# Kernel optimization log

Measured on AMD Instinct MI355X. Metric: run time of the kernel, lower is better.

The kernel has to match this reference:

```python
import jax, jax.numpy as jnp
import numpy as np

N, L, H, D = 4, 2048, 16, 32   # batch, seq len, heads, projection_dim
DIM = H * D                     # 512 model dim


def setup_inputs() -> dict:
    rng = jax.random.key(0)
    k1, k2, k3, k4, k5 = jax.random.split(rng, 5)
    query = jax.random.normal(k1, (N, L, DIM), dtype=jnp.float32)
    key = jax.random.normal(k2, (N, L, DIM), dtype=jnp.float32)
    scale = 0.02
    Wq = jax.random.normal(k3, (DIM, DIM), dtype=jnp.float32) * scale
    Wk = jax.random.normal(k4, (DIM, DIM), dtype=jnp.float32) * scale
    Wv = jax.random.normal(k5, (DIM, DIM), dtype=jnp.float32) * scale
    return {"query": query, "key": key, "Wq": Wq, "Wk": Wk, "Wv": Wv, "mask": 1}


def reference(query, key, Wq, Wk, Wv, mask):
    # torch Linear(bias=False): y = x @ W^T
    n, Lq, _ = query.shape
    _, Lk, _ = key.shape
    q = (query @ Wq.T).reshape(n, Lq, H, D).transpose(0, 2, 1, 3)  # (N,H,Lq,D)
    k = (key @ Wk.T).reshape(n, Lk, H, D).transpose(0, 2, 1, 3)    # (N,H,Lk,D)
    v = (key @ Wv.T).reshape(n, Lk, H, D).transpose(0, 2, 1, 3)    # (N,H,Lk,D)
    q = jax.nn.softmax(q, axis=-1)
    k = jax.nn.softmax(k, axis=-1)
    # causal branch (mask truthy): Lq*Lk > D^2*Lk, so the module takes the
    # cumsum-of-outer-products ("right") path:
    #   right = cumsum_l( k_l outer v_l );  out_l = q_l @ right_l
    kv = jnp.einsum('nhld,nhle->nhlde', k, v)   # (N,H,Lk,D,D) outer products
    S = jnp.cumsum(kv, axis=2)                  # running prefix state
    out = jnp.einsum('nhld,nhlde->nhle', q, S)  # (N,H,Lq,D)
    return out.transpose(0, 2, 1, 3).reshape(n, Lq, H * D)
```

## Files before the change

kernel.cpp:

```cpp
#include <hip/hip_runtime.h>

#define NB      4
#define L_SEQ   2048
#define H_HEADS 16
#define D32     32
#define DIM     512
#define NH      (NB * H_HEADS)
#define CHUNK   64
#define NCHUNK  (L_SEQ / CHUNK)

typedef __attribute__((ext_vector_type(8))) short bf16x8;
typedef __attribute__((ext_vector_type(4))) float f32x4;

__device__ __forceinline__ unsigned short f2bf(float x) {
    unsigned u = __float_as_uint(x);
    u += 0x7fff + ((u >> 16) & 1);
    return (unsigned short)(u >> 16);
}
__device__ __forceinline__ unsigned pack2(float lo, float hi) {
    return (unsigned)f2bf(lo) | ((unsigned)f2bf(hi) << 16);
}

#define QN  4194304
#define WN  262144
#define TOT (2*QN + 3*WN)
__global__ __launch_bounds__(256) void convert_kernel(
    const float* __restrict__ query, const float* __restrict__ key,
    const float* __restrict__ Wq, const float* __restrict__ Wk,
    const float* __restrict__ Wv, unsigned short* __restrict__ dst)
{
    int idx = (blockIdx.x * 256 + threadIdx.x) * 8;
    const float* src; int off;
    if (idx < QN)               { src = query; off = idx; }
    else if (idx < 2*QN)        { src = key;   off = idx - QN; }
    else if (idx < 2*QN + WN)   { src = Wq;    off = idx - 2*QN; }
    else if (idx < 2*QN + 2*WN) { src = Wk;    off = idx - 2*QN - WN; }
    else                        { src = Wv;    off = idx - 2*QN - 2*WN; }
    float4 a = *(const float4*)(src + off);
    float4 b = *(const float4*)(src + off + 4);
    *(uint4*)(dst + idx) = make_uint4(pack2(a.x, a.y), pack2(a.z, a.w),
                                      pack2(b.x, b.y), pack2(b.z, b.w));
}

#define GLL(g, l) __builtin_amdgcn_global_load_lds( \
    (const __attribute__((address_space(1))) unsigned int*)(g), \
    (__attribute__((address_space(3))) unsigned int*)(l), 16, 0, 0)

__global__ __launch_bounds__(256) void gemm3_mfma_kernel(
    const unsigned short* __restrict__ qb, const unsigned short* __restrict__ kb2,
    const unsigned short* __restrict__ wqb, const unsigned short* __restrict__ wkb,
    const unsigned short* __restrict__ wvb,
    unsigned short* __restrict__ Qs, unsigned short* __restrict__ Ks,
    unsigned short* __restrict__ Vt)
{
    const int z  = blockIdx.z;
    const int bx = blockIdx.x >> 6;
    const int by = blockIdx.x & 63;
    const unsigned short *PA, *PB;
    int m0, n0;
    if (z == 0)      { PA = qb;  PB = wqb; m0 = by*128; n0 = bx*128; }
    else if (z == 1) { PA = kb2; PB = wkb; m0 = by*128; n0 = bx*128; }
    else             { PA = wvb; PB = kb2; m0 = bx*128; n0 = by*128; }

    __shared__ unsigned short Asm[3 * 4096];
    __shared__ unsigned short Bsm[3 * 4096];

    const int t    = threadIdx.x;
    const int w    = t >> 6;
    const int lane = t & 63;
    const int wm   = w >> 1, wn = w & 1;
    const int lm   = lane & 15, quad = lane >> 4;

    const int qswz = quad ^ ((lm >> 1) & 3);
    const int aoff = (wm * 64 + lm) * 32 + qswz * 8;
    const int boff = (wn * 64 + lm) * 32 + qswz * 8;

    const int li0 = t, li1 = t + 256;
    const int row0 = li0 >> 2, row1 = li1 >> 2;
    const int qs0 = (li0 & 3) ^ ((li0 >> 3) & 3);
    const int qs1 = (li1 & 3) ^ ((li1 >> 3) & 3);
    const unsigned short* gA0 = PA + (size_t)(m0 + row0) * DIM + qs0 * 8;
    const unsigned short* gA1 = PA + (size_t)(m0 + row1) * DIM + qs1 * 8;
    const unsigned short* gB0 = PB + (size_t)(n0 + row0) * DIM + qs0 * 8;
    const unsigned short* gB1 = PB + (size_t)(n0 + row1) * DIM + qs1 * 8;

    f32x4 acc[4][4] = {};

#define STAGE(buf, kb) do { \
    GLL(gA0 + (kb), Asm + (buf) * 4096 + li0 * 8); \
    GLL(gB0 + (kb), Bsm + (buf) * 4096 + li0 * 8); \
    GLL(gA1 + (kb), Asm + (buf) * 4096 + li1 * 8); \
    GLL(gB1 + (kb), Bsm + (buf) * 4096 + li1 * 8); \
} while (0)

    STAGE(0, 0);
    STAGE(1, 32);
    __builtin_amdgcn_sched_barrier(0);
    asm volatile("s_waitcnt vmcnt(4)" ::: "memory");
    __builtin_amdgcn_s_barrier();
    __builtin_amdgcn_sched_barrier(0);

    #pragma unroll
    for (int step = 0; step < 16; ++step) {
        const int cur = step % 3;
        if (step < 14) STAGE((step + 2) % 3, (step + 2) * 32);
        const unsigned short* As = Asm + cur * 4096;
        const unsigned short* Bs = Bsm + cur * 4096;
        bf16x8 af[4], bfr[4];
        #pragma unroll
        for (int i = 0; i < 4; i++)
            af[i] = *(const bf16x8*)(As + aoff + i * 512);
        #pragma unroll
        for (int j = 0; j < 4; j++)
            bfr[j] = *(const bf16x8*)(Bs + boff + j * 512);
        #pragma unroll
        for (int i = 0; i < 4; i++)
            #pragma unroll
            for (int j = 0; j < 4; j++)
                acc[i][j] = __builtin_amdgcn_mfma_f32_16x16x32_bf16(
                    af[i], bfr[j], acc[i][j], 0, 0, 0);
        __builtin_amdgcn_sched_barrier(0);
        if (step < 14)       asm volatile("s_waitcnt vmcnt(4)" ::: "memory");
        else if (step == 14) asm volatile("s_waitcnt vmcnt(0)" ::: "memory");
        if (step < 15) {
            __builtin_amdgcn_s_barrier();
            __builtin_amdgcn_sched_barrier(0);
        }
    }
#undef STAGE

    if (z < 2) {
        #pragma unroll
        for (int i = 0; i < 4; i++)
            #pragma unroll
            for (int jp = 0; jp < 2; jp++)
                #pragma unroll
                for (int r = 0; r < 4; r++) {
                    float a = acc[i][2 * jp][r], b = acc[i][2 * jp + 1][r];
                    float m = fmaxf(a, b);
                    #pragma unroll
                    for (int off = 1; off < 16; off <<= 1)
                        m = fmaxf(m, __shfl_xor(m, off, 64));
                    float ea = __expf(a - m), eb = __expf(b - m);
                    float s = ea + eb;
                    #pragma unroll
                    for (int off = 1; off < 16; off <<= 1)
                        s += __shfl_xor(s, off, 64);
                    float inv = 1.0f / s;
                    acc[i][2 * jp][r]     = ea * inv;
                    acc[i][2 * jp + 1][r] = eb * inv;
                }
    }

    #pragma unroll
    for (int i = 0; i < 4; i++) {
        int rbase = m0 + wm * 64 + i * 16 + quad * 4;
        #pragma unroll
        for (int r = 0; r < 4; r++) {
            int rg = rbase + r;
            #pragma unroll
            for (int j = 0; j < 4; j++) {
                int cg = n0 + wn * 64 + j * 16 + lm;
                unsigned short val = f2bf(acc[i][j][r]);
                if (z < 2) {
                    int n = rg >> 11, l = rg & 2047;
                    int h = cg >> 5,  e = cg & 31;
                    unsigned short* dp = (z == 0) ? Qs : Ks;
                    dp[(((size_t)(n * H_HEADS + h)) * L_SEQ + l) * D32 + e] = val;
                } else {
                    int h = rg >> 5,  e = rg & 31;
                    int n = cg >> 11, l = cg & 2047;
                    Vt[(((size_t)(n * H_HEADS + h)) * D32 + e) * L_SEQ + l] = val;
                }
            }
        }
    }
}

__global__ __launch_bounds__(64) void chunk_kv_mfma_kernel(
    const unsigned short* __restrict__ Ks, const unsigned short* __restrict__ Vt,
    float* __restrict__ ckvT)
{
    const int c = blockIdx.x, nh = blockIdx.y;
    const int lane = threadIdx.x;
    const int lm = lane & 15, quad = lane >> 4;

    __shared__ unsigned short Kl[64 * 36];

    {
        const unsigned short* kg = Ks + ((size_t)nh * L_SEQ + c * CHUNK + lane) * D32;
        #pragma unroll
        for (int i = 0; i < 4; i++) {
            uint4 v = *(const uint4*)(kg + i * 8);
            *(uint4*)(Kl + lane * 36 + i * 8) = v;
        }
    }
    __syncthreads();

    f32x4 acc[2][2] = {};
    #pragma unroll
    for (int ch = 0; ch < 2; ch++) {
        bf16x8 aV[2], bK[2];
        #pragma unroll
        for (int mt = 0; mt < 2; mt++)
            aV[mt] = *(const bf16x8*)(Vt + ((size_t)nh * D32 + mt * 16 + lm) * L_SEQ
                                         + c * CHUNK + ch * 32 + quad * 8);
        #pragma unroll
        for (int nt = 0; nt < 2; nt++) {
            const unsigned short* kp = Kl + (ch * 32 + quad * 8) * 36 + nt * 16 + lm;
            #pragma unroll
            for (int j = 0; j < 8; j++) bK[nt][j] = (short)kp[j * 36];
        }
        #pragma unroll
        for (int mt = 0; mt < 2; mt++)
            #pragma unroll
            for (int nt = 0; nt < 2; nt++)
                acc[mt][nt] = __builtin_amdgcn_mfma_f32_16x16x32_bf16(
                    aV[mt], bK[nt], acc[mt][nt], 0, 0, 0);
    }
    #pragma unroll
    for (int mt = 0; mt < 2; mt++)
        #pragma unroll
        for (int nt = 0; nt < 2; nt++)
            #pragma unroll
            for (int r = 0; r < 4; r++) {
                int e = mt * 16 + quad * 4 + r;
                int d = nt * 16 + lm;
                ckvT[(((size_t)nh * NCHUNK + c) * 32 + e) * 32 + d] = acc[mt][nt][r];
            }
}

__global__ __launch_bounds__(64) void prefix_kernel(
    const float* __restrict__ ckvT, unsigned short* __restrict__ SpT)
{
    int nh   = blockIdx.y;
    int slot = blockIdx.x * 64 + threadIdx.x;
    const float* base = ckvT + (size_t)nh * NCHUNK * 1024 + slot * 4;
    unsigned short* sp = SpT + (size_t)nh * NCHUNK * 1024 + slot * 4;
    float4 acc = make_float4(0.f, 0.f, 0.f, 0.f);
    #pragma unroll
    for (int cb = 0; cb < NCHUNK; cb += 8) {
        float4 v[8];
        #pragma unroll
        for (int j = 0; j < 8; j++)
            v[j] = *(const float4*)(base + (size_t)(cb + j) * 1024);
        #pragma unroll
        for (int j = 0; j < 8; j++) {
            ushort4 u;
            u.x = f2bf(acc.x); u.y = f2bf(acc.y);
            u.z = f2bf(acc.z); u.w = f2bf(acc.w);
            *(ushort4*)(sp + (size_t)(cb + j) * 1024) = u;
            acc.x += v[j].x; acc.y += v[j].y;
            acc.z += v[j].z; acc.w += v[j].w;
        }
    }
}

__global__ __launch_bounds__(64) void chunk_out_mfma_kernel(
    const unsigned short* __restrict__ Qs, const unsigned short* __restrict__ Ks,
    const unsigned short* __restrict__ Vt, const unsigned short* __restrict__ SpT,
    float* __restrict__ out)
{
    const int c = blockIdx.x, nh = blockIdx.y;
    __shared__ unsigned short P[64 * 72];

    const int lane = threadIdx.x;
    const int lm = lane & 15, quad = lane >> 4;

    bf16x8 aQ[4], bK[4];
    #pragma unroll
    for (int i = 0; i < 4; i++)
        aQ[i] = *(const bf16x8*)(Qs + ((size_t)nh * L_SEQ + c * CHUNK + i * 16 + lm) * D32
                                    + quad * 8);
    #pragma unroll
    for (int j = 0; j < 4; j++)
        bK[j] = *(const bf16x8*)(Ks + ((size_t)nh * L_SEQ + c * CHUNK + j * 16 + lm) * D32
                                    + quad * 8);

    #pragma unroll
    for (int i = 0; i < 4; i++) {
        #pragma unroll
        for (int j = 0; j < 4; j++) {
            f32x4 p = {};
            if (j <= i) {
                p = __builtin_amdgcn_mfma_f32_16x16x32_bf16(aQ[i], bK[j], p, 0, 0, 0);
                if (j == i) {
                    #pragma unroll
                    for (int r = 0; r < 4; r++)
                        if (lm > quad * 4 + r) p[r] = 0.f;
                }
            }
            #pragma unroll
            for (int r = 0; r < 4; r++)
                P[(i * 16 + quad * 4 + r) * 72 + j * 16 + lm] = f2bf(p[r]);
        }
    }
    __syncthreads();

    bf16x8 bS[2], bV[2][2];
    #pragma unroll
    for (int nt = 0; nt < 2; nt++) {
        bS[nt] = *(const bf16x8*)(SpT + (((size_t)nh * NCHUNK + c) * 32 + nt * 16 + lm) * 32
                                      + quad * 8);
        #pragma unroll
        for (int ch = 0; ch < 2; ch++)
            bV[nt][ch] = *(const bf16x8*)(Vt + ((size_t)nh * D32 + nt * 16 + lm) * L_SEQ
                                             + c * CHUNK + ch * 32 + quad * 8);
    }

    const int n = nh >> 4, h = nh & 15;
    #pragma unroll
    for (int i = 0; i < 4; i++) {
        const int chmax = (i >> 1) + 1;
        bf16x8 aP[2];
        for (int ch = 0; ch < chmax; ch++)
            aP[ch] = *(const bf16x8*)&P[(i * 16 + lm) * 72 + ch * 32 + quad * 8];
        #pragma unroll
        for (int nt = 0; nt < 2; nt++) {
            f32x4 acc = {};
            acc = __builtin_amdgcn_mfma_f32_16x16x32_bf16(aQ[i], bS[nt], acc, 0, 0, 0);
            for (int ch = 0; ch < chmax; ch++)
                acc = __builtin_amdgcn_mfma_f32_16x16x32_bf16(aP[ch], bV[nt][ch], acc, 0, 0, 0);
            #pragma unroll
            for (int r = 0; r < 4; r++) {
                int lg = c * CHUNK + i * 16 + quad * 4 + r;
                out[((size_t)n * L_SEQ + lg) * DIM + h * D32 + nt * 16 + lm] = acc[r];
            }
        }
    }
}

extern "C" void kernel_launch(void* const* d_in, const int* in_sizes, int n_in,
                              void* d_out, int out_size, void* d_ws, size_t ws_size,
                              hipStream_t stream)
{
    (void)in_sizes; (void)n_in; (void)out_size; (void)ws_size;
    const float* query = (const float*)d_in[0];
    const float* key   = (const float*)d_in[1];
    const float* Wq    = (const float*)d_in[2];
    const float* Wk    = (const float*)d_in[3];
    const float* Wv    = (const float*)d_in[4];
    float* out = (float*)d_out;

    unsigned short* bf = (unsigned short*)d_ws;
    unsigned short* qb  = bf;
    unsigned short* kb  = qb + QN;
    unsigned short* wqb = kb + QN;
    unsigned short* wkb = wqb + WN;
    unsigned short* wvb = wkb + WN;
    unsigned short* Qs  = wvb + WN;
    const size_t SZ = (size_t)NH * L_SEQ * D32;
    unsigned short* Ks  = Qs + SZ;
    unsigned short* Vt  = Ks + SZ;
    unsigned short* SpT = Vt + SZ;
    float* ckvT = (float*)(SpT + (size_t)NH * NCHUNK * 1024);

    convert_kernel<<<dim3(TOT / (256 * 8)), dim3(256), 0, stream>>>(
        query, key, Wq, Wk, Wv, qb);
    gemm3_mfma_kernel<<<dim3(256, 1, 3), dim3(256), 0, stream>>>(
        qb, kb, wqb, wkb, wvb, Qs, Ks, Vt);
    chunk_kv_mfma_kernel<<<dim3(NCHUNK, NH), dim3(64), 0, stream>>>(Ks, Vt, ckvT);
    prefix_kernel<<<dim3(4, NH), dim3(64), 0, stream>>>(ckvT, SpT);
    chunk_out_mfma_kernel<<<dim3(NCHUNK, NH), dim3(64), 0, stream>>>(Qs, Ks, Vt, SpT, out);
}
```

Baseline: 138.3 us.

## Fuse fp32-to-bf16 activation conversion into the projection GEMM loader

The separate conversion pass no longer converts query and key to bf16. The projection GEMM now loads fp32 activations into registers, packs them to bf16 and writes them to swizzled LDS, while the weight operand still streams through direct global-to-LDS loads. This removes a full read and write of the bf16 activation copies plus most of the convert kernel's work. In exchange the GEMM reads twice the activation bytes per tile, holds more registers, and adds VALU packing and LDS stores to its pipeline. Because the V projection reuses key as its B operand, key is also read in fp32 three ways across z-blocks.

```diff
diff --git a/kernel.cpp b/kernel.cpp
--- a/kernel.cpp
+++ b/kernel.cpp
@@ -20,26 +20,26 @@
 __device__ __forceinline__ unsigned pack2(float lo, float hi) {
     return (unsigned)f2bf(lo) | ((unsigned)f2bf(hi) << 16);
 }
+__device__ __forceinline__ uint4 pack8(float4 a, float4 b) {
+    return make_uint4(pack2(a.x, a.y), pack2(a.z, a.w),
+                      pack2(b.x, b.y), pack2(b.z, b.w));
+}
 
 #define QN  4194304
 #define WN  262144
-#define TOT (2*QN + 3*WN)
+#define WTOT (3*WN)
 __global__ __launch_bounds__(256) void convert_kernel(
-    const float* __restrict__ query, const float* __restrict__ key,
     const float* __restrict__ Wq, const float* __restrict__ Wk,
     const float* __restrict__ Wv, unsigned short* __restrict__ dst)
 {
     int idx = (blockIdx.x * 256 + threadIdx.x) * 8;
     const float* src; int off;
-    if (idx < QN)               { src = query; off = idx; }
-    else if (idx < 2*QN)        { src = key;   off = idx - QN; }
-    else if (idx < 2*QN + WN)   { src = Wq;    off = idx - 2*QN; }
-    else if (idx < 2*QN + 2*WN) { src = Wk;    off = idx - 2*QN - WN; }
-    else                        { src = Wv;    off = idx - 2*QN - 2*WN; }
+    if (idx < WN)          { src = Wq; off = idx; }
+    else if (idx < 2*WN)   { src = Wk; off = idx - WN; }
+    else                   { src = Wv; off = idx - 2*WN; }
     float4 a = *(const float4*)(src + off);
     float4 b = *(const float4*)(src + off + 4);
-    *(uint4*)(dst + idx) = make_uint4(pack2(a.x, a.y), pack2(a.z, a.w),
-                                      pack2(b.x, b.y), pack2(b.z, b.w));
+    *(uint4*)(dst + idx) = pack8(a, b);
 }
 
 #define GLL(g, l) __builtin_amdgcn_global_load_lds( \
@@ -47,7 +47,7 @@
     (__attribute__((address_space(3))) unsigned int*)(l), 16, 0, 0)
 
 __global__ __launch_bounds__(256) void gemm3_mfma_kernel(
-    const unsigned short* __restrict__ qb, const unsigned short* __restrict__ kb2,
+    const float* __restrict__ query, const float* __restrict__ key,
     const unsigned short* __restrict__ wqb, const unsigned short* __restrict__ wkb,
     const unsigned short* __restrict__ wvb,
     unsigned short* __restrict__ Qs, unsigned short* __restrict__ Ks,
@@ -56,14 +56,19 @@
     const int z  = blockIdx.z;
     const int bx = blockIdx.x >> 6;
     const int by = blockIdx.x & 63;
-    const unsigned short *PA, *PB;
     int m0, n0;
-    if (z == 0)      { PA = qb;  PB = wqb; m0 = by*128; n0 = bx*128; }
-    else if (z == 1) { PA = kb2; PB = wkb; m0 = by*128; n0 = bx*128; }
-    else             { PA = wvb; PB = kb2; m0 = bx*128; n0 = by*128; }
+    if (z < 2) { m0 = by * 128; n0 = bx * 128; }
+    else       { m0 = bx * 128; n0 = by * 128; }
+
+    const float* fsrc = (z == 0) ? query : key;
+    const unsigned short* bsrc = (z == 0) ? wqb : (z == 1) ? wkb : wvb;
+    const int frb = (z < 2) ? m0 : n0;
+    const int brb = (z < 2) ? n0 : m0;
 
     __shared__ unsigned short Asm[3 * 4096];
     __shared__ unsigned short Bsm[3 * 4096];
+    unsigned short* fl = (z < 2) ? Asm : Bsm;
+    unsigned short* bl = (z < 2) ? Bsm : Asm;
 
     const int t    = threadIdx.x;
     const int w    = t >> 6;
@@ -76,58 +81,85 @@
     const int boff = (wn * 64 + lm) * 32 + qswz * 8;
 
     const int li0 = t, li1 = t + 256;
-    const int row0 = li0 >> 2, row1 = li1 >> 2;
-    const int qs0 = (li0 & 3) ^ ((li0 >> 3) & 3);
-    const int qs1 = (li1 & 3) ^ ((li1 >> 3) & 3);
-    const unsigned short* gA0 = PA + (size_t)(m0 + row0) * DIM + qs0 * 8;
-    const unsigned short* gA1 = PA + (size_t)(m0 + row1) * DIM + qs1 * 8;
-    const unsigned short* gB0 = PB + (size_t)(n0 + row0) * DIM + qs0 * 8;
-    const unsigned short* gB1 = PB + (size_t)(n0 + row1) * DIM + qs1 * 8;
+    const int row0 = li0 >> 2, q0 = li0 & 3;
+    const int row1 = li1 >> 2, q1 = li1 & 3;
+    const int sw0 = (row0 >> 1) & 3, sw1 = (row1 >> 1) & 3;
+    const float* f0 = fsrc + (size_t)(frb + row0) * DIM + q0 * 8;
+    const float* f1 = fsrc + (size_t)(frb + row1) * DIM + q1 * 8;
+    const int fd0 = (row0 * 4 + (q0 ^ sw0)) * 8;
+    const int fd1 = (row1 * 4 + (q1 ^ sw1)) * 8;
+    const unsigned short* g0 = bsrc + (size_t)(brb + row0) * DIM + (q0 ^ sw0) * 8;
+    const unsigned short* g1 = bsrc + (size_t)(brb + row1) * DIM + (q1 ^ sw1) * 8;
 
     f32x4 acc[4][4] = {};
-
-#define STAGE(buf, kb) do { \
-    GLL(gA0 + (kb), Asm + (buf) * 4096 + li0 * 8); \
-    GLL(gB0 + (kb), Bsm + (buf) * 4096 + li0 * 8); \
-    GLL(gA1 + (kb), Asm + (buf) * 4096 + li1 * 8); \
-    GLL(gB1 + (kb), Bsm + (buf) * 4096 + li1 * 8); \
+    float4 Pa0[2], Pa1[2], Pb0[2], Pb1[2];
+
+#define FLOAD(s, kb) do { \
+    Pa0[s] = *(const float4*)(f0 + (kb));     Pa1[s] = *(const float4*)(f0 + (kb) + 4); \
+    Pb0[s] = *(const float4*)(f1 + (kb));     Pb1[s] = *(const float4*)(f1 + (kb) + 4); \
 } while (0)
-
-    STAGE(0, 0);
-    STAGE(1, 32);
+#define FWRITE(s, buf) do { \
+    *(uint4*)(fl + (buf) * 4096 + fd0) = pack8(Pa0[s], Pa1[s]); \
+    *(uint4*)(fl + (buf) * 4096 + fd1) = pack8(Pb0[s], Pb1[s]); \
+} while (0)
+#define GSTAGE(buf, kb) do { \
+    GLL(g0 + (kb), bl + (buf) * 4096 + li0 * 8); \
+    GLL(g1 + (kb), bl + (buf) * 4096 + li1 * 8); \
+} while (0)
+
+    FLOAD(0, 0);
+    GSTAGE(0, 0);
+    FLOAD(1, 32);
+    GSTAGE(1, 32);
     __builtin_amdgcn_sched_barrier(0);
-    asm volatile("s_waitcnt vmcnt(4)" ::: "memory");
+    asm volatile("s_waitcnt vmcnt(8)" ::: "memory");
+    FWRITE(0, 0);
+    __builtin_amdgcn_sched_barrier(0);
+    asm volatile("s_waitcnt vmcnt(6)" ::: "memory");
+    asm volatile("s_waitcnt lgkmcnt(0)" ::: "memory");
     __builtin_amdgcn_s_barrier();
     __builtin_amdgcn_sched_barrier(0);
 
     #pragma unroll
     for (int step = 0; step < 16; ++step) {
         const int cur = step % 3;
-        if (step < 14) STAGE((step + 2) % 3, (step + 2) * 32);
-        const unsigned short* As = Asm + cur * 4096;
-        const unsigned short* Bs = Bsm + cur * 4096;
-        bf16x8 af[4], bfr[4];
-        #pragma unroll
-        for (int i = 0; i < 4; i++)
-            af[i] = *(const bf16x8*)(As + aoff + i * 512);
-        #pragma unroll
-        for (int j = 0; j < 4; j++)
-            bfr[j] = *(const bf16x8*)(Bs + boff + j * 512);
-        #pragma unroll
-        for (int i = 0; i < 4; i++)
+        if (step < 14) FLOAD(step & 1, (step + 2) * 32);
+        __builtin_amdgcn_sched_barrier(0);
+        if (step < 14)       asm volatile("s_waitcnt vmcnt(6)" ::: "memory");
+        else if (step == 14) asm volatile("s_waitcnt vmcnt(2)" ::: "memory");
+        if (step < 15) FWRITE((step + 1) & 1, (step + 1) % 3);
+        __builtin_amdgcn_sched_barrier(0);
+        if (step < 14) GSTAGE((step + 2) % 3, (step + 2) * 32);
+        __builtin_amdgcn_sched_barrier(0);
+        {
+            const unsigned short* As = Asm + cur * 4096;
+            const unsigned short* Bs = Bsm + cur * 4096;
+            bf16x8 af[4], bfr[4];
+            #pragma unroll
+            for (int i = 0; i < 4; i++)
+                af[i] = *(const bf16x8*)(As + aoff + i * 512);
             #pragma unroll
             for (int j = 0; j < 4; j++)
-                acc[i][j] = __builtin_amdgcn_mfma_f32_16x16x32_bf16(
-                    af[i], bfr[j], acc[i][j], 0, 0, 0);
+                bfr[j] = *(const bf16x8*)(Bs + boff + j * 512);
+            #pragma unroll
+            for (int i = 0; i < 4; i++)
+                #pragma unroll
+                for (int j = 0; j < 4; j++)
+                    acc[i][j] = __builtin_amdgcn_mfma_f32_16x16x32_bf16(
+                        af[i], bfr[j], acc[i][j], 0, 0, 0);
+        }
         __builtin_amdgcn_sched_barrier(0);
-        if (step < 14)       asm volatile("s_waitcnt vmcnt(4)" ::: "memory");
+        if (step < 14)       asm volatile("s_waitcnt vmcnt(6)" ::: "memory");
         else if (step == 14) asm volatile("s_waitcnt vmcnt(0)" ::: "memory");
         if (step < 15) {
+            asm volatile("s_waitcnt lgkmcnt(0)" ::: "memory");
             __builtin_amdgcn_s_barrier();
             __builtin_amdgcn_sched_barrier(0);
         }
     }
-#undef STAGE
+#undef FLOAD
+#undef FWRITE
+#undef GSTAGE
 
     if (z < 2) {
         #pragma unroll
@@ -343,9 +375,7 @@
     float* out = (float*)d_out;
 
     unsigned short* bf = (unsigned short*)d_ws;
-    unsigned short* qb  = bf;
-    unsigned short* kb  = qb + QN;
-    unsigned short* wqb = kb + QN;
+    unsigned short* wqb = bf;
     unsigned short* wkb = wqb + WN;
     unsigned short* wvb = wkb + WN;
     unsigned short* Qs  = wvb + WN;
@@ -355,10 +385,10 @@
     unsigned short* SpT = Vt + SZ;
     float* ckvT = (float*)(SpT + (size_t)NH * NCHUNK * 1024);
 
-    convert_kernel<<<dim3(TOT / (256 * 8)), dim3(256), 0, stream>>>(
-        query, key, Wq, Wk, Wv, qb);
+    convert_kernel<<<dim3(WTOT / (256 * 8)), dim3(256), 0, stream>>>(
+        Wq, Wk, Wv, wqb);
     gemm3_mfma_kernel<<<dim3(256, 1, 3), dim3(256), 0, stream>>>(
-        qb, kb, wqb, wkb, wvb, Qs, Ks, Vt);
+        query, key, wqb, wkb, wvb, Qs, Ks, Vt);
     chunk_kv_mfma_kernel<<<dim3(NCHUNK, NH), dim3(64), 0, stream>>>(Ks, Vt, ckvT);
     prefix_kernel<<<dim3(4, NH), dim3(64), 0, stream>>>(ckvT, SpT);
     chunk_out_mfma_kernel<<<dim3(NCHUNK, NH), dim3(64), 0, stream>>>(Qs, Ks, Vt, SpT, out);
```

After: 138.3 us. About the same (-0.0%).

## Fuse K and V projections into one GEMM sharing the key A-tile

Applied to the files above, without the earlier changes.

The z=1 blocks of the projection GEMM now compute both key@Wk^T and key@Wv^T from the same staged key tile, with two accumulator sets and a second B buffer in LDS. This removes the separate z=2 pass and the reload of the key matrix. The V output is now computed untransposed and written as packed 4-element stores into the transposed layout, replacing scalar stores. In exchange, register pressure and LDS use rise: two 4x4 accumulator sets plus a third triple-buffered tile, with a launch bound of 2 blocks per CU. The z=0 and z=1 blocks also become unbalanced in work.

```diff
diff --git a/kernel.cpp b/kernel.cpp
--- a/kernel.cpp
+++ b/kernel.cpp
@@ -42,11 +42,56 @@
                                       pack2(b.x, b.y), pack2(b.z, b.w));
 }
 
+__device__ __forceinline__ void softmax_heads(f32x4 (&acc)[4][4]) {
+    #pragma unroll
+    for (int i = 0; i < 4; i++)
+        #pragma unroll
+        for (int jp = 0; jp < 2; jp++)
+            #pragma unroll
+            for (int r = 0; r < 4; r++) {
+                float a = acc[i][2 * jp][r], b = acc[i][2 * jp + 1][r];
+                float m = fmaxf(a, b);
+                #pragma unroll
+                for (int off = 1; off < 16; off <<= 1)
+                    m = fmaxf(m, __shfl_xor(m, off, 64));
+                float ea = __expf(a - m), eb = __expf(b - m);
+                float s = ea + eb;
+                #pragma unroll
+                for (int off = 1; off < 16; off <<= 1)
+                    s += __shfl_xor(s, off, 64);
+                float inv = 1.0f / s;
+                acc[i][2 * jp][r]     = ea * inv;
+                acc[i][2 * jp + 1][r] = eb * inv;
+            }
+}
+
+__device__ __forceinline__ void scatter_qk(
+    const f32x4 (&acc)[4][4], unsigned short* __restrict__ dp,
+    int m0, int n0, int wm, int wn, int quad, int lm)
+{
+    #pragma unroll
+    for (int i = 0; i < 4; i++) {
+        int rbase = m0 + wm * 64 + i * 16 + quad * 4;
+        #pragma unroll
+        for (int r = 0; r < 4; r++) {
+            int rg = rbase + r;
+            int n = rg >> 11, l = rg & 2047;
+            #pragma unroll
+            for (int j = 0; j < 4; j++) {
+                int cg = n0 + wn * 64 + j * 16 + lm;
+                int h = cg >> 5, e = cg & 31;
+                dp[(((size_t)(n * H_HEADS + h)) * L_SEQ + l) * D32 + e] =
+                    f2bf(acc[i][j][r]);
+            }
+        }
+    }
+}
+
 #define GLL(g, l) __builtin_amdgcn_global_load_lds( \
     (const __attribute__((address_space(1))) unsigned int*)(g), \
     (__attribute__((address_space(3))) unsigned int*)(l), 16, 0, 0)
 
-__global__ __launch_bounds__(256) void gemm3_mfma_kernel(
+__global__ __launch_bounds__(256, 2) void gemm3_mfma_kernel(
     const unsigned short* __restrict__ qb, const unsigned short* __restrict__ kb2,
     const unsigned short* __restrict__ wqb, const unsigned short* __restrict__ wkb,
     const unsigned short* __restrict__ wvb,
@@ -56,14 +101,14 @@
     const int z  = blockIdx.z;
     const int bx = blockIdx.x >> 6;
     const int by = blockIdx.x & 63;
-    const unsigned short *PA, *PB;
-    int m0, n0;
-    if (z == 0)      { PA = qb;  PB = wqb; m0 = by*128; n0 = bx*128; }
-    else if (z == 1) { PA = kb2; PB = wkb; m0 = by*128; n0 = bx*128; }
-    else             { PA = wvb; PB = kb2; m0 = bx*128; n0 = by*128; }
+    const int m0 = by * 128, n0 = bx * 128;
+
+    const unsigned short* PA  = z ? kb2 : qb;
+    const unsigned short* PB1 = z ? wkb : wqb;
 
     __shared__ unsigned short Asm[3 * 4096];
-    __shared__ unsigned short Bsm[3 * 4096];
+    __shared__ unsigned short B1sm[3 * 4096];
+    __shared__ unsigned short B2sm[3 * 4096];
 
     const int t    = threadIdx.x;
     const int w    = t >> 6;
@@ -79,99 +124,124 @@
     const int row0 = li0 >> 2, row1 = li1 >> 2;
     const int qs0 = (li0 & 3) ^ ((li0 >> 3) & 3);
     const int qs1 = (li1 & 3) ^ ((li1 >> 3) & 3);
-    const unsigned short* gA0 = PA + (size_t)(m0 + row0) * DIM + qs0 * 8;
-    const unsigned short* gA1 = PA + (size_t)(m0 + row1) * DIM + qs1 * 8;
-    const unsigned short* gB0 = PB + (size_t)(n0 + row0) * DIM + qs0 * 8;
-    const unsigned short* gB1 = PB + (size_t)(n0 + row1) * DIM + qs1 * 8;
-
-    f32x4 acc[4][4] = {};
-
-#define STAGE(buf, kb) do { \
-    GLL(gA0 + (kb), Asm + (buf) * 4096 + li0 * 8); \
-    GLL(gB0 + (kb), Bsm + (buf) * 4096 + li0 * 8); \
-    GLL(gA1 + (kb), Asm + (buf) * 4096 + li1 * 8); \
-    GLL(gB1 + (kb), Bsm + (buf) * 4096 + li1 * 8); \
+    const unsigned short* gA0 = PA  + (size_t)(m0 + row0) * DIM + qs0 * 8;
+    const unsigned short* gA1 = PA  + (size_t)(m0 + row1) * DIM + qs1 * 8;
+    const unsigned short* gB10 = PB1 + (size_t)(n0 + row0) * DIM + qs0 * 8;
+    const unsigned short* gB11 = PB1 + (size_t)(n0 + row1) * DIM + qs1 * 8;
+
+    if (z == 0) {
+        f32x4 acc[4][4] = {};
+#define STG0(buf, kb) do { \
+        GLL(gA0  + (kb), Asm  + (buf) * 4096 + li0 * 8); \
+        GLL(gB10 + (kb), B1sm + (buf) * 4096 + li0 * 8); \
+        GLL(gA1  + (kb), Asm  + (buf) * 4096 + li1 * 8); \
+        GLL(gB11 + (kb), B1sm + (buf) * 4096 + li1 * 8); \
 } while (0)
-
-    STAGE(0, 0);
-    STAGE(1, 32);
-    __builtin_amdgcn_sched_barrier(0);
-    asm volatile("s_waitcnt vmcnt(4)" ::: "memory");
-    __builtin_amdgcn_s_barrier();
-    __builtin_amdgcn_sched_barrier(0);
-
-    #pragma unroll
-    for (int step = 0; step < 16; ++step) {
-        const int cur = step % 3;
-        if (step < 14) STAGE((step + 2) % 3, (step + 2) * 32);
-        const unsigned short* As = Asm + cur * 4096;
-        const unsigned short* Bs = Bsm + cur * 4096;
-        bf16x8 af[4], bfr[4];
-        #pragma unroll
-        for (int i = 0; i < 4; i++)
-            af[i] = *(const bf16x8*)(As + aoff + i * 512);
-        #pragma unroll
-        for (int j = 0; j < 4; j++)
-            bfr[j] = *(const bf16x8*)(Bs + boff + j * 512);
-        #pragma unroll
-        for (int i = 0; i < 4; i++)
+        STG0(0, 0);
+        STG0(1, 32);
+        __builtin_amdgcn_sched_barrier(0);
+        asm volatile("s_waitcnt vmcnt(4)" ::: "memory");
+        __builtin_amdgcn_s_barrier();
+        __builtin_amdgcn_sched_barrier(0);
+
+        #pragma unroll
+        for (int step = 0; step < 16; ++step) {
+            const int cur = step % 3;
+            if (step < 14) STG0((step + 2) % 3, (step + 2) * 32);
+            const unsigned short* As = Asm + cur * 4096;
+            const unsigned short* Bs = B1sm + cur * 4096;
+            bf16x8 af[4], bf1[4];
+            #pragma unroll
+            for (int i = 0; i < 4; i++)
+                af[i] = *(const bf16x8*)(As + aoff + i * 512);
             #pragma unroll
             for (int j = 0; j < 4; j++)
-                acc[i][j] = __builtin_amdgcn_mfma_f32_16x16x32_bf16(
-                    af[i], bfr[j], acc[i][j], 0, 0, 0);
+                bf1[j] = *(const bf16x8*)(Bs + boff + j * 512);
+            #pragma unroll
+            for (int i = 0; i < 4; i++)
+                #pragma unroll
+                for (int j = 0; j < 4; j++)
+                    acc[i][j] = __builtin_amdgcn_mfma_f32_16x16x32_bf16(
+                        af[i], bf1[j], acc[i][j], 0, 0, 0);
+            __builtin_amdgcn_sched_barrier(0);
+            if (step < 14)       asm volatile("s_waitcnt vmcnt(4)" ::: "memory");
+            else if (step == 14) asm volatile("s_waitcnt vmcnt(0)" ::: "memory");
+            if (step < 15) {
+                __builtin_amdgcn_s_barrier();
+                __builtin_amdgcn_sched_barrier(0);
+            }
+        }
+#undef STG0
+        softmax_heads(acc);
+        scatter_qk(acc, Qs, m0, n0, wm, wn, quad, lm);
+    } else {
+        const unsigned short* gB20 = wvb + (size_t)(n0 + row0) * DIM + qs0 * 8;
+        const unsigned short* gB21 = wvb + (size_t)(n0 + row1) * DIM + qs1 * 8;
+        f32x4 acc[4][4] = {};
+        f32x4 acc2[4][4] = {};
+#define STG1(buf, kb) do { \
+        GLL(gA0  + (kb), Asm  + (buf) * 4096 + li0 * 8); \
+        GLL(gB10 + (kb), B1sm + (buf) * 4096 + li0 * 8); \
+        GLL(gB20 + (kb), B2sm + (buf) * 4096 + li0 * 8); \
+        GLL(gA1  + (kb), Asm  + (buf) * 4096 + li1 * 8); \
+        GLL(gB11 + (kb), B1sm + (buf) * 4096 + li1 * 8); \
+        GLL(gB21 + (kb), B2sm + (buf) * 4096 + li1 * 8); \
+} while (0)
+        STG1(0, 0);
+        STG1(1, 32);
         __builtin_amdgcn_sched_barrier(0);
-        if (step < 14)       asm volatile("s_waitcnt vmcnt(4)" ::: "memory");
-        else if (step == 14) asm volatile("s_waitcnt vmcnt(0)" ::: "memory");
-        if (step < 15) {
-            __builtin_amdgcn_s_barrier();
+        asm volatile("s_waitcnt vmcnt(6)" ::: "memory");
+        __builtin_amdgcn_s_barrier();
+        __builtin_amdgcn_sched_barrier(0);
+
+        #pragma unroll
+        for (int step = 0; step < 16; ++step) {
+            const int cur = step % 3;
+            if (step < 14) STG1((step + 2) % 3, (step + 2) * 32);
+            const unsigned short* As  = Asm  + cur * 4096;
+            const unsigned short* B1s = B1sm + cur * 4096;
+            const unsigned short* B2s = B2sm + cur * 4096;
+            bf16x8 af[4], bf1[4], bf2[4];
+            #pragma unroll
+            for (int i = 0; i < 4; i++)
+                af[i] = *(const bf16x8*)(As + aoff + i * 512);
+            #pragma unroll
+            for (int j = 0; j < 4; j++) {
+                bf1[j] = *(const bf16x8*)(B1s + boff + j * 512);
+                bf2[j] = *(const bf16x8*)(B2s + boff + j * 512);
+            }
+            #pragma unroll
+            for (int i = 0; i < 4; i++)
+                #pragma unroll
+                for (int j = 0; j < 4; j++) {
+                    acc[i][j]  = __builtin_amdgcn_mfma_f32_16x16x32_bf16(
+                        af[i], bf1[j], acc[i][j], 0, 0, 0);
+                    acc2[i][j] = __builtin_amdgcn_mfma_f32_16x16x32_bf16(
+                        af[i], bf2[j], acc2[i][j], 0, 0, 0);
+                }
             __builtin_amdgcn_sched_barrier(0);
-        }
-    }
-#undef STAGE
-
-    if (z < 2) {
-        #pragma unroll
-        for (int i = 0; i < 4; i++)
-            #pragma unroll
-            for (int jp = 0; jp < 2; jp++)
-                #pragma unroll
-                for (int r = 0; r < 4; r++) {
-                    float a = acc[i][2 * jp][r], b = acc[i][2 * jp + 1][r];
-                    float m = fmaxf(a, b);
-                    #pragma unroll
-                    for (int off = 1; off < 16; off <<= 1)
-                        m = fmaxf(m, __shfl_xor(m, off, 64));
-                    float ea = __expf(a - m), eb = __expf(b - m);
-                    float s = ea + eb;
-                    #pragma unroll
-                    for (int off = 1; off < 16; off <<= 1)
-                        s += __shfl_xor(s, off, 64);
-                    float inv = 1.0f / s;
-                    acc[i][2 * jp][r]     = ea * inv;
-                    acc[i][2 * jp + 1][r] = eb * inv;
-                }
-    }
-
-    #pragma unroll
-    for (int i = 0; i < 4; i++) {
-        int rbase = m0 + wm * 64 + i * 16 + quad * 4;
-        #pragma unroll
-        for (int r = 0; r < 4; r++) {
-            int rg = rbase + r;
+            if (step < 14)       asm volatile("s_waitcnt vmcnt(6)" ::: "memory");
+            else if (step == 14) asm volatile("s_waitcnt vmcnt(0)" ::: "memory");
+            if (step < 15) {
+                __builtin_amdgcn_s_barrier();
+                __builtin_amdgcn_sched_barrier(0);
+            }
+        }
+#undef STG1
+        softmax_heads(acc);
+        scatter_qk(acc, Ks, m0, n0, wm, wn, quad, lm);
+        #pragma unroll
+        for (int i = 0; i < 4; i++) {
+            int lg0 = m0 + wm * 64 + i * 16 + quad * 4;
+            int nb = lg0 >> 11, ll = lg0 & 2047;
             #pragma unroll
             for (int j = 0; j < 4; j++) {
                 int cg = n0 + wn * 64 + j * 16 + lm;
-                unsigned short val = f2bf(acc[i][j][r]);
-                if (z < 2) {
-                    int n = rg >> 11, l = rg & 2047;
-                    int h = cg >> 5,  e = cg & 31;
-                    unsigned short* dp = (z == 0) ? Qs : Ks;
-                    dp[(((size_t)(n * H_HEADS + h)) * L_SEQ + l) * D32 + e] = val;
-                } else {
-                    int h = rg >> 5,  e = rg & 31;
-                    int n = cg >> 11, l = cg & 2047;
-                    Vt[(((size_t)(n * H_HEADS + h)) * D32 + e) * L_SEQ + l] = val;
-                }
+                int h = cg >> 5, e = cg & 31;
+                ushort4 u;
+                u.x = f2bf(acc2[i][j][0]); u.y = f2bf(acc2[i][j][1]);
+                u.z = f2bf(acc2[i][j][2]); u.w = f2bf(acc2[i][j][3]);
+                *(ushort4*)(Vt + (((size_t)(nb * H_HEADS + h)) * D32 + e) * L_SEQ + ll) = u;
             }
         }
     }
@@ -357,7 +427,7 @@
 
     convert_kernel<<<dim3(TOT / (256 * 8)), dim3(256), 0, stream>>>(
         query, key, Wq, Wk, Wv, qb);
-    gemm3_mfma_kernel<<<dim3(256, 1, 3), dim3(256), 0, stream>>>(
+    gemm3_mfma_kernel<<<dim3(256, 1, 2), dim3(256), 0, stream>>>(
         qb, kb, wqb, wkb, wvb, Qs, Ks, Vt);
     chunk_kv_mfma_kernel<<<dim3(NCHUNK, NH), dim3(64), 0, stream>>>(Ks, Vt, ckvT);
     prefix_kernel<<<dim3(4, NH), dim3(64), 0, stream>>>(ckvT, SpT);
```

New measurement: 133.6 us (median of 2 runs). -3.4%, faster.
